# Kernel optimization log

Measured on AMD Instinct MI355X. Metric: run time of the kernel, lower is better.

The kernel has to match this reference:

```python
import jax, jax.numpy as jnp
import numpy as np

B, T, C, HS = 256, 256, 384, 64

def setup_inputs() -> dict:
    key = jax.random.key(0)
    k1, k2, k3, k4 = jax.random.split(key, 4)
    s = 1.0 / np.sqrt(C)  # Linear-like init scale
    return {
        "x": jax.random.normal(k1, (B, T, C), dtype=jnp.float32),
        "Wq": jax.random.normal(k2, (C, HS), dtype=jnp.float32) * s,
        "Wk": jax.random.normal(k3, (C, HS), dtype=jnp.float32) * s,
        "Wv": jax.random.normal(k4, (C, HS), dtype=jnp.float32) * s,
    }

def reference(x, Wq, Wk, Wv):
    # q,k,v: [B,T,HS]
    q = jnp.einsum("btc,ch->bth", x, Wq)
    k = jnp.einsum("btc,ch->bth", x, Wk)
    v = jnp.einsum("btc,ch->bth", x, Wv)
    scale = k.shape[-1] ** -0.5
    scores = jnp.einsum("bth,bsh->bts", q, k) * scale  # [B,T,T]
    causal = jnp.tril(jnp.ones((x.shape[1], x.shape[1]), dtype=bool))
    scores = jnp.where(causal, scores, -jnp.inf)
    attn = jax.nn.softmax(scores, axis=-1)
    # dropout omitted (eval mode / deterministic reference)
    return jnp.einsum("bts,bsh->bth", attn, v)
```

## Files before the change

### kernel.cpp

```cpp
#include <hip/hip_runtime.h>
#include <hip/hip_bf16.h>

#define NB 256
#define NT 256
#define NC 384
#define NH 64
#define NW 192
#define WT_ELEMS (NW * NC)

typedef short bf16x8 __attribute__((ext_vector_type(8)));
typedef float f32x4 __attribute__((ext_vector_type(4)));

__device__ __forceinline__ unsigned short f2bf(float f) {
  union { float f; unsigned int i; } c;
  c.f = f;
  const unsigned int r = c.i + 0x7fffu + ((c.i >> 16) & 1u);
  return (unsigned short)(r >> 16);
}

__device__ __forceinline__ unsigned short f2bf_hw(float f) {
  __hip_bfloat16 b = __float2bfloat16(f);
  return *reinterpret_cast<unsigned short*>(&b);
}

__device__ __forceinline__ bf16x8 cvt8(float4 lo, float4 hi) {
  union { bf16x8 v; unsigned short u[8]; } au;
  au.u[0] = f2bf_hw(lo.x); au.u[1] = f2bf_hw(lo.y);
  au.u[2] = f2bf_hw(lo.z); au.u[3] = f2bf_hw(lo.w);
  au.u[4] = f2bf_hw(hi.x); au.u[5] = f2bf_hw(hi.y);
  au.u[6] = f2bf_hw(hi.z); au.u[7] = f2bf_hw(hi.w);
  return au.v;
}

__global__ __launch_bounds__(256) void w_prep_kernel(
    const float* __restrict__ Wq,
    const float* __restrict__ Wk,
    const float* __restrict__ Wv,
    unsigned short* __restrict__ Wt2) {
  const int o = blockIdx.x * 256 + threadIdx.x;
  if (o >= WT_ELEMS) return;
  const int j = o & 7;
  const int lane = (o >> 3) & 63;
  const int fi = o >> 9;
  const int ni = fi % 12;
  const int kt = fi / 12;
  const int n = ni * 16 + (lane & 15);
  const int k = kt * 32 + ((lane >> 4) << 3) + j;
  const float* W = (n < 64) ? Wq : (n < 128) ? Wk : Wv;
  Wt2[o] = f2bf(W[k * NH + (n & 63)]);
}

__global__ __launch_bounds__(512, 2) void fused_qkv_attn_kernel(
    const float* __restrict__ x,
    const unsigned short* __restrict__ Wt2,
    float* __restrict__ out) {
  __shared__ __align__(16) unsigned char lds[147456];

  const int tid = threadIdx.x;
  const int w = tid >> 6;
  const int lane = tid & 63;
  const int l15 = lane & 15;
  const int lg = lane >> 4;
  const int b = blockIdx.x;
  const int row0 = b * NT;
  const int qt = (w < 4) ? w : 11 - w;
  const int wbase = qt * 32;

  f32x4 acc[2][12];
#pragma unroll
  for (int mi = 0; mi < 2; ++mi)
#pragma unroll
    for (int ni = 0; ni < 12; ++ni)
#pragma unroll
      for (int r = 0; r < 4; ++r) acc[mi][ni][r] = 0.f;

#pragma unroll
  for (int i = 0; i < 18; ++i) {
    const int idx = i * 512 + tid;
    __builtin_amdgcn_global_load_lds(
        (const __attribute__((address_space(1))) void*)(Wt2 + idx * 8),
        (__attribute__((address_space(3))) void*)(lds + idx * 16), 16, 0, 0);
  }

  const float* xa0 = x + (size_t)(row0 + wbase + l15) * NC + lg * 8;
  const float* xa1 = xa0 + (size_t)16 * NC;

  float4 aA0, aA1, aA2, aA3, aB0, aB1, aB2, aB3, aC0, aC1, aC2, aC3;

#define LOADA(S, KT)                                                          \
  do {                                                                        \
    a##S##0 = *reinterpret_cast<const float4*>(xa0 + (KT)*32);                \
    a##S##1 = *reinterpret_cast<const float4*>(xa0 + (KT)*32 + 4);            \
    a##S##2 = *reinterpret_cast<const float4*>(xa1 + (KT)*32);                \
    a##S##3 = *reinterpret_cast<const float4*>(xa1 + (KT)*32 + 4);            \
  } while (0)

  LOADA(A, 0);
  LOADA(B, 1);
  LOADA(C, 2);

  asm volatile("s_waitcnt vmcnt(12)" ::: "memory");
  __builtin_amdgcn_s_barrier();

  const unsigned short* Wl =
      reinterpret_cast<const unsigned short*>(lds) + lane * 8;

#define STEP(S, KT)                                                           \
  do {                                                                        \
    const bf16x8 afr0 = cvt8(a##S##0, a##S##1);                               \
    const bf16x8 afr1 = cvt8(a##S##2, a##S##3);                               \
    if ((KT) + 3 < 12) LOADA(S, (KT) + 3);                                    \
    _Pragma("unroll") for (int ni = 0; ni < 12; ++ni) {                       \
      const bf16x8 bfr = *reinterpret_cast<const bf16x8*>(                    \
          Wl + (size_t)((KT)*12 + ni) * 512);                                 \
      acc[0][ni] = __builtin_amdgcn_mfma_f32_16x16x32_bf16(                   \
          afr0, bfr, acc[0][ni], 0, 0, 0);                                    \
      acc[1][ni] = __builtin_amdgcn_mfma_f32_16x16x32_bf16(                   \
          afr1, bfr, acc[1][ni], 0, 0, 0);                                    \
    }                                                                         \
  } while (0)

  STEP(A, 0);  STEP(B, 1);  STEP(C, 2);
  STEP(A, 3);  STEP(B, 4);  STEP(C, 5);
  STEP(A, 6);  STEP(B, 7);  STEP(C, 8);
  STEP(A, 9);  STEP(B, 10); STEP(C, 11);

  __syncthreads();

  unsigned short* Kls = reinterpret_cast<unsigned short*>(lds);
  unsigned short* Vtls = reinterpret_cast<unsigned short*>(lds + 32768);
  unsigned short* Qls = reinterpret_cast<unsigned short*>(lds + 65536);
  unsigned short* Pls = reinterpret_cast<unsigned short*>(lds + 98304);

#pragma unroll
  for (int mi = 0; mi < 2; ++mi)
#pragma unroll
    for (int ni = 0; ni < 12; ++ni) {
      const int n = ni * 16 + l15;
#pragma unroll
      for (int r = 0; r < 4; ++r) {
        const int srow = wbase + mi * 16 + lg * 4 + r;
        const unsigned short val = f2bf_hw(acc[mi][ni][r]);
        if (ni < 4) {
          Qls[srow * 64 + (n ^ ((srow & 7) << 3))] = val;
        } else if (ni < 8) {
          const int h = n - 64;
          Kls[srow * 64 + (h ^ ((srow & 7) << 3))] = val;
        } else {
          const int h = n - 128;
          Vtls[h * 256 + (srow ^ ((h & 7) << 3))] = val;
        }
      }
    }
  __syncthreads();

  const int q0 = wbase;
  bf16x8 a_q[2][2];
#pragma unroll
  for (int mi = 0; mi < 2; ++mi)
#pragma unroll
    for (int ks = 0; ks < 2; ++ks) {
      const int srow = q0 + mi * 16 + l15;
      a_q[mi][ks] = *reinterpret_cast<const bf16x8*>(
          Qls + srow * 64 + ((ks * 32 + lg * 8) ^ ((srow & 7) << 3)));
    }

  f32x4 o[2][4];
  float mrun[2][4], lrun[2][4];
#pragma unroll
  for (int mi = 0; mi < 2; ++mi)
#pragma unroll
    for (int r = 0; r < 4; ++r) {
      mrun[mi][r] = -3.0e38f;
      lrun[mi][r] = 0.f;
#pragma unroll
      for (int hi = 0; hi < 4; ++hi) o[mi][hi][r] = 0.f;
    }

  unsigned short* Pw = Pls + w * 1280;

  for (int j = 0; j <= qt; ++j) {
    f32x4 s_acc[2][2];
#pragma unroll
    for (int mi = 0; mi < 2; ++mi)
#pragma unroll
      for (int si = 0; si < 2; ++si)
#pragma unroll
        for (int r = 0; r < 4; ++r) s_acc[mi][si][r] = 0.f;

#pragma unroll
    for (int ks = 0; ks < 2; ++ks) {
      bf16x8 bk[2];
#pragma unroll
      for (int si = 0; si < 2; ++si) {
        const int srow = j * 32 + si * 16 + l15;
        const int kel = ks * 32 + lg * 8;
        bk[si] = *reinterpret_cast<const bf16x8*>(
            Kls + srow * 64 + (kel ^ ((srow & 7) << 3)));
      }
#pragma unroll
      for (int mi = 0; mi < 2; ++mi)
#pragma unroll
        for (int si = 0; si < 2; ++si)
          s_acc[mi][si] = __builtin_amdgcn_mfma_f32_16x16x32_bf16(
              a_q[mi][ks], bk[si], s_acc[mi][si], 0, 0, 0);
    }

    const bool diag = (j == qt);
#pragma unroll
    for (int mi = 0; mi < 2; ++mi) {
#pragma unroll
      for (int r = 0; r < 4; ++r) {
        const int mloc = mi * 16 + lg * 4 + r;
        float v0 = s_acc[mi][0][r] * 0.125f;
        float v1 = s_acc[mi][1][r] * 0.125f;
        if (diag) {
          if (l15 > mloc) v0 = -3.0e38f;
          if (16 + l15 > mloc) v1 = -3.0e38f;
        }
        float pm = fmaxf(v0, v1);
        pm = fmaxf(pm, __shfl_xor(pm, 1, 16));
        pm = fmaxf(pm, __shfl_xor(pm, 2, 16));
        pm = fmaxf(pm, __shfl_xor(pm, 4, 16));
        pm = fmaxf(pm, __shfl_xor(pm, 8, 16));
        const float mnew = fmaxf(mrun[mi][r], pm);
        const float alpha = __expf(mrun[mi][r] - mnew);
        mrun[mi][r] = mnew;
        const float p0 = __expf(v0 - mnew);
        const float p1 = __expf(v1 - mnew);
        float ps = p0 + p1;
        ps += __shfl_xor(ps, 1, 16);
        ps += __shfl_xor(ps, 2, 16);
        ps += __shfl_xor(ps, 4, 16);
        ps += __shfl_xor(ps, 8, 16);
        lrun[mi][r] = lrun[mi][r] * alpha + ps;
#pragma unroll
        for (int hi = 0; hi < 4; ++hi) o[mi][hi][r] *= alpha;
        Pw[mloc * 40 + l15] = f2bf(p0);
        Pw[mloc * 40 + 16 + l15] = f2bf(p1);
      }
    }

    bf16x8 pa[2];
#pragma unroll
    for (int mt = 0; mt < 2; ++mt)
      pa[mt] = *reinterpret_cast<const bf16x8*>(
          Pw + (mt * 16 + l15) * 40 + lg * 8);
#pragma unroll
    for (int hi = 0; hi < 4; ++hi) {
      const int h = hi * 16 + l15;
      const int sel = j * 32 + lg * 8;
      const bf16x8 bv = *reinterpret_cast<const bf16x8*>(
          Vtls + h * 256 + (sel ^ ((h & 7) << 3)));
#pragma unroll
      for (int mt = 0; mt < 2; ++mt)
        o[mt][hi] = __builtin_amdgcn_mfma_f32_16x16x32_bf16(
            pa[mt], bv, o[mt][hi], 0, 0, 0);
    }
  }

  float* og = out + ((size_t)b * NT + q0) * NH;
#pragma unroll
  for (int mi = 0; mi < 2; ++mi)
#pragma unroll
    for (int r = 0; r < 4; ++r) {
      const float inv = 1.f / lrun[mi][r];
      const int m = mi * 16 + lg * 4 + r;
#pragma unroll
      for (int hi = 0; hi < 4; ++hi)
        og[m * 64 + hi * 16 + l15] = o[mi][hi][r] * inv;
    }
}

extern "C" void kernel_launch(void* const* d_in, const int* in_sizes, int n_in,
                              void* d_out, int out_size, void* d_ws,
                              size_t ws_size, hipStream_t stream) {
  const float* x  = (const float*)d_in[0];
  const float* Wq = (const float*)d_in[1];
  const float* Wk = (const float*)d_in[2];
  const float* Wv = (const float*)d_in[3];
  unsigned short* Wt2 = (unsigned short*)d_ws;
  float* out = (float*)d_out;

  w_prep_kernel<<<dim3((WT_ELEMS + 255) / 256), dim3(256), 0, stream>>>(
      Wq, Wk, Wv, Wt2);
  fused_qkv_attn_kernel<<<dim3(NB), dim3(512), 0, stream>>>(x, Wt2, out);
}
```

Before: 44.22 us.

## Split work across 16 waves with 16-row tiles per wave

Doubles the block size to 1024 threads, so each of the 16 waves owns 16 query rows instead of 32. A packed lookup table assigns row tiles to waves to balance causal work, and the diagonal masking now handles a 16-row tile inside a 32-key block. This adds latency hiding and shortens each wave's serial attention loop. In exchange there are more barriers per block and lower MFMA reuse per wave, and the 144KB LDS buffer still allows only one block per CU. The vmcnt wait becomes a full drain before the projection starts.

```diff
diff --git a/kernel.cpp b/kernel.cpp
--- a/kernel.cpp
+++ b/kernel.cpp
@@ -50,7 +50,7 @@
   Wt2[o] = f2bf(W[k * NH + (n & 63)]);
 }
 
-__global__ __launch_bounds__(512, 2) void fused_qkv_attn_kernel(
+__global__ __launch_bounds__(1024, 4) void fused_qkv_attn_kernel(
     const float* __restrict__ x,
     const unsigned short* __restrict__ Wt2,
     float* __restrict__ out) {
@@ -63,43 +63,39 @@
   const int lg = lane >> 4;
   const int b = blockIdx.x;
   const int row0 = b * NT;
-  const int qt = (w < 4) ? w : 11 - w;
-  const int wbase = qt * 32;
-
-  f32x4 acc[2][12];
-#pragma unroll
-  for (int mi = 0; mi < 2; ++mi)
-#pragma unroll
-    for (int ni = 0; ni < 12; ++ni)
-#pragma unroll
-      for (int r = 0; r < 4; ++r) acc[mi][ni][r] = 0.f;
-
-#pragma unroll
-  for (int i = 0; i < 18; ++i) {
-    const int idx = i * 512 + tid;
+  const int qt =
+      (int)((0x583E2F49C1A7B6D0ull >> (w << 2)) & 15ull);
+  const int wbase = qt * 16;
+
+  f32x4 acc[12];
+#pragma unroll
+  for (int ni = 0; ni < 12; ++ni)
+#pragma unroll
+    for (int r = 0; r < 4; ++r) acc[ni][r] = 0.f;
+
+#pragma unroll
+  for (int i = 0; i < 9; ++i) {
+    const int idx = i * 1024 + tid;
     __builtin_amdgcn_global_load_lds(
         (const __attribute__((address_space(1))) void*)(Wt2 + idx * 8),
         (__attribute__((address_space(3))) void*)(lds + idx * 16), 16, 0, 0);
   }
 
   const float* xa0 = x + (size_t)(row0 + wbase + l15) * NC + lg * 8;
-  const float* xa1 = xa0 + (size_t)16 * NC;
-
-  float4 aA0, aA1, aA2, aA3, aB0, aB1, aB2, aB3, aC0, aC1, aC2, aC3;
+
+  float4 aA0, aA1, aB0, aB1, aC0, aC1;
 
 #define LOADA(S, KT)                                                          \
   do {                                                                        \
     a##S##0 = *reinterpret_cast<const float4*>(xa0 + (KT)*32);                \
     a##S##1 = *reinterpret_cast<const float4*>(xa0 + (KT)*32 + 4);            \
-    a##S##2 = *reinterpret_cast<const float4*>(xa1 + (KT)*32);                \
-    a##S##3 = *reinterpret_cast<const float4*>(xa1 + (KT)*32 + 4);            \
   } while (0)
 
   LOADA(A, 0);
   LOADA(B, 1);
   LOADA(C, 2);
 
-  asm volatile("s_waitcnt vmcnt(12)" ::: "memory");
+  asm volatile("s_waitcnt vmcnt(0)" ::: "memory");
   __builtin_amdgcn_s_barrier();
 
   const unsigned short* Wl =
@@ -107,16 +103,13 @@
 
 #define STEP(S, KT)                                                           \
   do {                                                                        \
-    const bf16x8 afr0 = cvt8(a##S##0, a##S##1);                               \
-    const bf16x8 afr1 = cvt8(a##S##2, a##S##3);                               \
+    const bf16x8 afr = cvt8(a##S##0, a##S##1);                                \
     if ((KT) + 3 < 12) LOADA(S, (KT) + 3);                                    \
     _Pragma("unroll") for (int ni = 0; ni < 12; ++ni) {                       \
       const bf16x8 bfr = *reinterpret_cast<const bf16x8*>(                    \
           Wl + (size_t)((KT)*12 + ni) * 512);                                 \
-      acc[0][ni] = __builtin_amdgcn_mfma_f32_16x16x32_bf16(                   \
-          afr0, bfr, acc[0][ni], 0, 0, 0);                                    \
-      acc[1][ni] = __builtin_amdgcn_mfma_f32_16x16x32_bf16(                   \
-          afr1, bfr, acc[1][ni], 0, 0, 0);                                    \
+      acc[ni] = __builtin_amdgcn_mfma_f32_16x16x32_bf16(                      \
+          afr, bfr, acc[ni], 0, 0, 0);                                        \
     }                                                                         \
   } while (0)
 
@@ -133,60 +126,52 @@
   unsigned short* Pls = reinterpret_cast<unsigned short*>(lds + 98304);
 
 #pragma unroll
-  for (int mi = 0; mi < 2; ++mi)
-#pragma unroll
-    for (int ni = 0; ni < 12; ++ni) {
-      const int n = ni * 16 + l15;
-#pragma unroll
-      for (int r = 0; r < 4; ++r) {
-        const int srow = wbase + mi * 16 + lg * 4 + r;
-        const unsigned short val = f2bf_hw(acc[mi][ni][r]);
-        if (ni < 4) {
-          Qls[srow * 64 + (n ^ ((srow & 7) << 3))] = val;
-        } else if (ni < 8) {
-          const int h = n - 64;
-          Kls[srow * 64 + (h ^ ((srow & 7) << 3))] = val;
-        } else {
-          const int h = n - 128;
-          Vtls[h * 256 + (srow ^ ((h & 7) << 3))] = val;
-        }
+  for (int ni = 0; ni < 12; ++ni) {
+    const int n = ni * 16 + l15;
+#pragma unroll
+    for (int r = 0; r < 4; ++r) {
+      const int srow = wbase + lg * 4 + r;
+      const unsigned short val = f2bf_hw(acc[ni][r]);
+      if (ni < 4) {
+        Qls[srow * 64 + (n ^ ((srow & 7) << 3))] = val;
+      } else if (ni < 8) {
+        const int h = n - 64;
+        Kls[srow * 64 + (h ^ ((srow & 7) << 3))] = val;
+      } else {
+        const int h = n - 128;
+        Vtls[h * 256 + (srow ^ ((h & 7) << 3))] = val;
       }
     }
+  }
   __syncthreads();
 
-  const int q0 = wbase;
-  bf16x8 a_q[2][2];
-#pragma unroll
-  for (int mi = 0; mi < 2; ++mi)
-#pragma unroll
-    for (int ks = 0; ks < 2; ++ks) {
-      const int srow = q0 + mi * 16 + l15;
-      a_q[mi][ks] = *reinterpret_cast<const bf16x8*>(
-          Qls + srow * 64 + ((ks * 32 + lg * 8) ^ ((srow & 7) << 3)));
-    }
-
-  f32x4 o[2][4];
-  float mrun[2][4], lrun[2][4];
-#pragma unroll
-  for (int mi = 0; mi < 2; ++mi)
-#pragma unroll
-    for (int r = 0; r < 4; ++r) {
-      mrun[mi][r] = -3.0e38f;
-      lrun[mi][r] = 0.f;
-#pragma unroll
-      for (int hi = 0; hi < 4; ++hi) o[mi][hi][r] = 0.f;
-    }
-
-  unsigned short* Pw = Pls + w * 1280;
-
-  for (int j = 0; j <= qt; ++j) {
-    f32x4 s_acc[2][2];
-#pragma unroll
-    for (int mi = 0; mi < 2; ++mi)
-#pragma unroll
-      for (int si = 0; si < 2; ++si)
-#pragma unroll
-        for (int r = 0; r < 4; ++r) s_acc[mi][si][r] = 0.f;
+  bf16x8 a_q[2];
+#pragma unroll
+  for (int ks = 0; ks < 2; ++ks) {
+    const int srow = wbase + l15;
+    a_q[ks] = *reinterpret_cast<const bf16x8*>(
+        Qls + srow * 64 + ((ks * 32 + lg * 8) ^ ((srow & 7) << 3)));
+  }
+
+  f32x4 o[4];
+  float mrun[4], lrun[4];
+#pragma unroll
+  for (int r = 0; r < 4; ++r) {
+    mrun[r] = -3.0e38f;
+    lrun[r] = 0.f;
+#pragma unroll
+    for (int hi = 0; hi < 4; ++hi) o[hi][r] = 0.f;
+  }
+
+  unsigned short* Pw = Pls + w * 640;
+  const int njmax = qt >> 1;
+
+  for (int j = 0; j <= njmax; ++j) {
+    f32x4 s_acc[2];
+#pragma unroll
+    for (int si = 0; si < 2; ++si)
+#pragma unroll
+      for (int r = 0; r < 4; ++r) s_acc[si][r] = 0.f;
 
 #pragma unroll
     for (int ks = 0; ks < 2; ++ks) {
@@ -199,77 +184,68 @@
             Kls + srow * 64 + (kel ^ ((srow & 7) << 3)));
       }
 #pragma unroll
-      for (int mi = 0; mi < 2; ++mi)
-#pragma unroll
-        for (int si = 0; si < 2; ++si)
-          s_acc[mi][si] = __builtin_amdgcn_mfma_f32_16x16x32_bf16(
-              a_q[mi][ks], bk[si], s_acc[mi][si], 0, 0, 0);
-    }
-
-    const bool diag = (j == qt);
-#pragma unroll
-    for (int mi = 0; mi < 2; ++mi) {
-#pragma unroll
-      for (int r = 0; r < 4; ++r) {
-        const int mloc = mi * 16 + lg * 4 + r;
-        float v0 = s_acc[mi][0][r] * 0.125f;
-        float v1 = s_acc[mi][1][r] * 0.125f;
-        if (diag) {
+      for (int si = 0; si < 2; ++si)
+        s_acc[si] = __builtin_amdgcn_mfma_f32_16x16x32_bf16(
+            a_q[ks], bk[si], s_acc[si], 0, 0, 0);
+    }
+
+    const bool dlast = (j == njmax);
+#pragma unroll
+    for (int r = 0; r < 4; ++r) {
+      const int mloc = lg * 4 + r;
+      float v0 = s_acc[0][r] * 0.125f;
+      float v1 = s_acc[1][r] * 0.125f;
+      if (dlast) {
+        if ((qt & 1) == 0) {
           if (l15 > mloc) v0 = -3.0e38f;
-          if (16 + l15 > mloc) v1 = -3.0e38f;
+          v1 = -3.0e38f;
+        } else {
+          if (l15 > mloc) v1 = -3.0e38f;
         }
-        float pm = fmaxf(v0, v1);
-        pm = fmaxf(pm, __shfl_xor(pm, 1, 16));
-        pm = fmaxf(pm, __shfl_xor(pm, 2, 16));
-        pm = fmaxf(pm, __shfl_xor(pm, 4, 16));
-        pm = fmaxf(pm, __shfl_xor(pm, 8, 16));
-        const float mnew = fmaxf(mrun[mi][r], pm);
-        const float alpha = __expf(mrun[mi][r] - mnew);
-        mrun[mi][r] = mnew;
-        const float p0 = __expf(v0 - mnew);
-        const float p1 = __expf(v1 - mnew);
-        float ps = p0 + p1;
-        ps += __shfl_xor(ps, 1, 16);
-        ps += __shfl_xor(ps, 2, 16);
-        ps += __shfl_xor(ps, 4, 16);
-        ps += __shfl_xor(ps, 8, 16);
-        lrun[mi][r] = lrun[mi][r] * alpha + ps;
-#pragma unroll
-        for (int hi = 0; hi < 4; ++hi) o[mi][hi][r] *= alpha;
-        Pw[mloc * 40 + l15] = f2bf(p0);
-        Pw[mloc * 40 + 16 + l15] = f2bf(p1);
       }
-    }
-
-    bf16x8 pa[2];
-#pragma unroll
-    for (int mt = 0; mt < 2; ++mt)
-      pa[mt] = *reinterpret_cast<const bf16x8*>(
-          Pw + (mt * 16 + l15) * 40 + lg * 8);
+      float pm = fmaxf(v0, v1);
+      pm = fmaxf(pm, __shfl_xor(pm, 1, 16));
+      pm = fmaxf(pm, __shfl_xor(pm, 2, 16));
+      pm = fmaxf(pm, __shfl_xor(pm, 4, 16));
+      pm = fmaxf(pm, __shfl_xor(pm, 8, 16));
+      const float mnew = fmaxf(mrun[r], pm);
+      const float alpha = __expf(mrun[r] - mnew);
+      mrun[r] = mnew;
+      const float p0 = __expf(v0 - mnew);
+      const float p1 = __expf(v1 - mnew);
+      float ps = p0 + p1;
+      ps += __shfl_xor(ps, 1, 16);
+      ps += __shfl_xor(ps, 2, 16);
+      ps += __shfl_xor(ps, 4, 16);
+      ps += __shfl_xor(ps, 8, 16);
+      lrun[r] = lrun[r] * alpha + ps;
+#pragma unroll
+      for (int hi = 0; hi < 4; ++hi) o[hi][r] *= alpha;
+      Pw[mloc * 40 + l15] = f2bf(p0);
+      Pw[mloc * 40 + 16 + l15] = f2bf(p1);
+    }
+
+    const bf16x8 pa =
+        *reinterpret_cast<const bf16x8*>(Pw + l15 * 40 + lg * 8);
 #pragma unroll
     for (int hi = 0; hi < 4; ++hi) {
       const int h = hi * 16 + l15;
       const int sel = j * 32 + lg * 8;
       const bf16x8 bv = *reinterpret_cast<const bf16x8*>(
           Vtls + h * 256 + (sel ^ ((h & 7) << 3)));
-#pragma unroll
-      for (int mt = 0; mt < 2; ++mt)
-        o[mt][hi] = __builtin_amdgcn_mfma_f32_16x16x32_bf16(
-            pa[mt], bv, o[mt][hi], 0, 0, 0);
-    }
-  }
-
-  float* og = out + ((size_t)b * NT + q0) * NH;
-#pragma unroll
-  for (int mi = 0; mi < 2; ++mi)
-#pragma unroll
-    for (int r = 0; r < 4; ++r) {
-      const float inv = 1.f / lrun[mi][r];
-      const int m = mi * 16 + lg * 4 + r;
-#pragma unroll
-      for (int hi = 0; hi < 4; ++hi)
-        og[m * 64 + hi * 16 + l15] = o[mi][hi][r] * inv;
-    }
+      o[hi] = __builtin_amdgcn_mfma_f32_16x16x32_bf16(pa, bv, o[hi], 0, 0, 0);
+    }
+  }
+
+  float* og = out + ((size_t)b * NT + wbase) * NH;
+#pragma unroll
+  for (int r = 0; r < 4; ++r) {
+    const float inv = 1.f / lrun[r];
+    const int m = lg * 4 + r;
+#pragma unroll
+    for (int hi = 0; hi < 4; ++hi)
+      og[m * 64 + hi * 16 + l15] = o[hi][r] * inv;
+  }
 }
 
 extern "C" void kernel_launch(void* const* d_in, const int* in_sizes, int n_in,
@@ -284,5 +260,5 @@
 
   w_prep_kernel<<<dim3((WT_ELEMS + 255) / 256), dim3(256), 0, stream>>>(
       Wq, Wk, Wv, Wt2);
-  fused_qkv_attn_kernel<<<dim3(NB), dim3(512), 0, stream>>>(x, Wt2, out);
-}
+  fused_qkv_attn_kernel<<<dim3(NB), dim3(1024), 0, stream>>>(x, Wt2, out);
+}
```

Result: faster. 41.04 us, median of 2 (-7.2%).
